# Performance work log

Hardware: AMD Instinct MI355X
Metric: run time of the kernel (lower is better)

## Reference

```python
import jax, jax.numpy as jnp
import numpy as np

B, S, D = 4, 2048, 1024
NEG = -1e10

def setup_inputs() -> dict:
    key = jax.random.key(0)
    ks = jax.random.split(key, 8)
    scale = 1.0 / np.sqrt(D)
    return {
        "hidden_states": jax.random.normal(ks[0], (B, S, D), jnp.float32),
        "mask": jax.random.randint(ks[1], (B, S), 0, 2, jnp.int32),
        "Wq": jax.random.normal(ks[2], (D, D), jnp.float32) * scale,
        "bq": jnp.zeros((D,), jnp.float32),
        "Wk": jax.random.normal(ks[3], (D, D), jnp.float32) * scale,
        "bk": jnp.zeros((D,), jnp.float32),
        "Wv": jax.random.normal(ks[4], (D, D), jnp.float32) * scale,
        "bv": jnp.zeros((D,), jnp.float32),
        "Wo": jax.random.normal(ks[5], (D, D), jnp.float32) * scale,
        "bo": jnp.zeros((D,), jnp.float32),
    }

def reference(hidden_states, mask, Wq, bq, Wk, bk, Wv, bv, Wo, bo):
    # torch Linear: y = x @ W.T + b
    q = jnp.einsum('bsd,ed->bse', hidden_states, Wq) + bq
    k = jnp.einsum('bsd,ed->bse', hidden_states, Wk) + bk
    v = jnp.einsum('bsd,ed->bse', hidden_states, Wv) + bv
    inv_sqrt_d = jnp.asarray(int(hidden_states.shape[-1]) ** (-0.5), hidden_states.dtype)
    weight = jnp.einsum('bqd,bkd->bqk', q, k) * inv_sqrt_d  # [B,S,S]
    # mask viewed as [B,1,S]: key-padding mask broadcast over query dim
    m = mask.reshape(mask.shape[0], 1, mask.shape[1])
    weight = jnp.where(m == 0, jnp.asarray(NEG, weight.dtype), weight)
    a = jax.nn.softmax(weight, axis=-1)
    hid = jnp.einsum('bqk,bkd->bqd', a, v)
    hid_o = jnp.einsum('bsd,ed->bse', hid, Wo) + bo
    return hidden_states + hid_o  # residual=True
```

## Files before the change

### kernel.cpp

```cpp
#include <hip/hip_runtime.h>
#include <stdint.h>


typedef __attribute__((ext_vector_type(8))) short bf16x8;
typedef __attribute__((ext_vector_type(4))) float f32x4;

typedef __attribute__((address_space(3))) void lds_void_t;
typedef __attribute__((address_space(1))) const void glb_void_t;

__device__ __forceinline__ ushort f2bf(float f) {
  uint32_t u = __float_as_uint(f);
  u += 0x7FFF + ((u >> 16) & 1);
  return (ushort)(u >> 16);
}
__device__ __forceinline__ float bf2f(ushort u) {
  return __uint_as_float(((uint32_t)u) << 16);
}

__global__ __launch_bounds__(256) void convert_all(
    const float* __restrict__ X, const float* __restrict__ Wq,
    const float* __restrict__ Wk, const float* __restrict__ Wv,
    const float* __restrict__ Wo, const float* __restrict__ bq,
    const float* __restrict__ bk,
    ushort* __restrict__ Xb, ushort* __restrict__ Wqb, ushort* __restrict__ Wkb,
    ushort* __restrict__ Wvb, ushort* __restrict__ Wob,
    float* __restrict__ bqk) {
  if (blockIdx.x >= 12288) {
#pragma unroll
    for (int u = 0; u < 2; ++u) {
      int idx4 = threadIdx.x * 2 + u;
      int base = idx4 * 4;
      float4 v = (base < 1024) ? *(const float4*)(bq + base)
                               : *(const float4*)(bk + base - 1024);
      *(float4*)(bqk + base) = v;
    }
    return;
  }
  int64_t i = (int64_t)blockIdx.x * blockDim.x + threadIdx.x;
  int64_t o4 = i * 4;
  const float* s; ushort* d; int64_t off;
  if (o4 < 8388608)        { s = X;  d = Xb;  off = o4; }
  else if (o4 < 9437184)   { s = Wq; d = Wqb; off = o4 - 8388608; }
  else if (o4 < 10485760)  { s = Wk; d = Wkb; off = o4 - 9437184; }
  else if (o4 < 11534336)  { s = Wv; d = Wvb; off = o4 - 10485760; }
  else                     { s = Wo; d = Wob; off = o4 - 11534336; }
  float4 v = *(const float4*)(s + off);
  ushort4 o;
  o.x = f2bf(v.x); o.y = f2bf(v.y); o.z = f2bf(v.z); o.w = f2bf(v.w);
  *(ushort4*)(d + off) = o;
}


#define BAR   __builtin_amdgcn_s_barrier()
#define SCHED __builtin_amdgcn_sched_barrier(0)
#define LGKM0 asm volatile("s_waitcnt lgkmcnt(0)" ::: "memory")
#define VMC(n) asm volatile("s_waitcnt vmcnt(" #n ")" ::: "memory")

#define ST(gp, loff, BUFBASE)                                                  \
  do {                                                                         \
    __builtin_amdgcn_global_load_lds((glb_void_t*)(gp),                        \
                                     (lds_void_t*)((BUFBASE) + (loff)), 16, 0, 0); \
    (gp) += 64;                                                                \
  } while (0)

template <int MODE>
__global__ __launch_bounds__(512, 2) void gemm8(
    const ushort* __restrict__ Ag, const ushort* __restrict__ Bg,
    void* __restrict__ Og, const float* __restrict__ bias,
    const float* __restrict__ resid,
    int N, int K, int lda, int ldb, int ldo,
    long long sAz, long long sBz, long long sOz, float scale) {
  __shared__ ushort As0[16384], As1[16384], Bs0[8192], Bs1[8192];

  const int z = blockIdx.z;
  const ushort* A = Ag + (int64_t)z * sAz;
  const ushort* B = Bg + (int64_t)z * sBz;

  const int tilesN = N >> 7;
  const int nwg = gridDim.x;
  const int q8 = nwg >> 3, r8 = nwg & 7;
  const int xcd = blockIdx.x & 7, sub = blockIdx.x >> 3;
  const int wg = (xcd < r8 ? xcd * (q8 + 1) : r8 * (q8 + 1) + (xcd - r8) * q8) + sub;
  const int tm = wg / tilesN, tn = wg % tilesN;

  const int tid = threadIdx.x;
  const int wid = tid >> 6;
  const int lane = tid & 63;
  const int lr = lane & 15;
  const int kq = lane >> 4;
  const int wr = (wid >> 1) * 64;
  const int wc = (wid & 1) * 64;

  const int64_t abase = (int64_t)tm * 256;
  const int64_t bbase = (int64_t)tn * 128;

  const int idxA0 = tid, idxA1 = 512 + tid, idxA2 = 1024 + tid, idxA3 = 1536 + tid;
  const int idxB0 = tid, idxB1 = 512 + tid;

  const int rA0 = idxA0 >> 3, rA1 = idxA1 >> 3, rA2 = idxA2 >> 3, rA3 = idxA3 >> 3;
  const int rB0 = idxB0 >> 3, rB1 = idxB1 >> 3;

  const ushort* gA0 = A + (abase + rA0) * lda + ((idxA0 & 7) ^ (rA0 & 7)) * 8;
  const ushort* gA1 = A + (abase + rA1) * lda + ((idxA1 & 7) ^ (rA1 & 7)) * 8;
  const ushort* gA2 = A + (abase + rA2) * lda + ((idxA2 & 7) ^ (rA2 & 7)) * 8;
  const ushort* gA3 = A + (abase + rA3) * lda + ((idxA3 & 7) ^ (rA3 & 7)) * 8;
  const ushort* gB0 = B + (bbase + rB0) * ldb + ((idxB0 & 7) ^ (rB0 & 7)) * 8;
  const ushort* gB1 = B + (bbase + rB1) * ldb + ((idxB1 & 7) ^ (rB1 & 7)) * 8;

  const int lA0 = idxA0 * 8, lA1 = idxA1 * 8, lA2 = idxA2 * 8, lA3 = idxA3 * 8;
  const int lB0 = idxB0 * 8, lB1 = idxB1 * 8;

  const int rsw0 = (kq ^ (lr & 7)) * 8;
  const int rsw1 = rsw0 ^ 32;
  const ushort* Arp0 = As0 + (wr + lr) * 64;
  const ushort* Arp1 = As1 + (wr + lr) * 64;
  const ushort* Brp0 = Bs0 + (wc + lr) * 64;
  const ushort* Brp1 = Bs1 + (wc + lr) * 64;

  bf16x8 a[4][2], b[4][2];
  f32x4 acc[4][4];
#pragma unroll
  for (int m = 0; m < 4; ++m)
#pragma unroll
    for (int n = 0; n < 4; ++n) acc[m][n] = (f32x4){0.f, 0.f, 0.f, 0.f};

#define RD_A(BUF, mi)                                                    \
  {                                                                      \
    const ushort* p_ = (BUF ? Arp1 : Arp0) + (mi) * 1024;                \
    a[mi][0] = *(const bf16x8*)(p_ + rsw0);                              \
    a[mi][1] = *(const bf16x8*)(p_ + rsw1);                              \
  }
#define RD_B(BUF, ni)                                                    \
  {                                                                      \
    const ushort* p_ = (BUF ? Brp1 : Brp0) + (ni) * 1024;                \
    b[ni][0] = *(const bf16x8*)(p_ + rsw0);                              \
    b[ni][1] = *(const bf16x8*)(p_ + rsw1);                              \
  }
#define MFMA2(mi, ni)                                                                   \
  acc[mi][ni] = __builtin_amdgcn_mfma_f32_16x16x32_bf16(a[mi][0], b[ni][0], acc[mi][ni], 0, 0, 0); \
  acc[mi][ni] = __builtin_amdgcn_mfma_f32_16x16x32_bf16(a[mi][1], b[ni][1], acc[mi][ni], 0, 0, 0);
#define QUAD(m0_, n0_)                                                   \
  __builtin_amdgcn_s_setprio(1);                                         \
  MFMA2(m0_, n0_) MFMA2(m0_, n0_ + 1) MFMA2(m0_ + 1, n0_) MFMA2(m0_ + 1, n0_ + 1) \
  __builtin_amdgcn_s_setprio(0);

  ST(gA0, lA0, As0); ST(gA1, lA1, As0); ST(gA2, lA2, As0); ST(gA3, lA3, As0);
  ST(gB0, lB0, Bs0); ST(gB1, lB1, Bs0);
  ST(gA0, lA0, As1); ST(gA1, lA1, As1); ST(gA2, lA2, As1); ST(gA3, lA3, As1);
  ST(gB0, lB0, Bs1); ST(gB1, lB1, Bs1);
  VMC(6); BAR; SCHED;

  const int NI = K >> 7;
  for (int i = 0; i < NI; ++i) {
    const bool last = (i == NI - 1);
    RD_A(0, 0) RD_A(0, 1) RD_B(0, 0) RD_B(0, 1)
    BAR; LGKM0; SCHED;
    QUAD(0, 0)
    SCHED; BAR;
    RD_B(0, 2) RD_B(0, 3)
    BAR; LGKM0; SCHED;
    QUAD(0, 2)
    SCHED; BAR;
    RD_A(0, 2) RD_A(0, 3)
    BAR; LGKM0; SCHED;
    QUAD(2, 2)
    SCHED; BAR;
    if (!last) { ST(gA0, lA0, As0); ST(gA1, lA1, As0); }
    BAR; SCHED;
    QUAD(2, 0)
    SCHED;
    if (last) { VMC(0); } else { VMC(2); }
    BAR;
    RD_A(1, 0) RD_A(1, 1) RD_B(1, 0) RD_B(1, 1)
    if (!last) { ST(gA2, lA2, As0); ST(gA3, lA3, As0); }
    BAR; LGKM0; SCHED;
    QUAD(0, 0)
    SCHED; BAR;
    RD_A(1, 2) RD_A(1, 3) RD_B(1, 2) RD_B(1, 3)
    if (!last) { ST(gB0, lB0, Bs0); ST(gB1, lB1, Bs0); }
    BAR; LGKM0; SCHED;
    QUAD(0, 2)
    SCHED; BAR;
    if (!last) { ST(gA0, lA0, As1); ST(gA1, lA1, As1); ST(gA2, lA2, As1); ST(gA3, lA3, As1); }
    BAR; SCHED;
    QUAD(2, 2)
    SCHED; BAR;
    if (!last) { ST(gB0, lB0, Bs1); ST(gB1, lB1, Bs1); }
    BAR; SCHED;
    QUAD(2, 0)
    SCHED;
    if (!last) { VMC(6); }
    BAR;
  }

#pragma unroll
  for (int m = 0; m < 4; ++m) {
#pragma unroll
    for (int n = 0; n < 4; ++n) {
      int c = tn * 128 + wc + n * 16 + lr;
      int r0 = tm * 256 + wr + m * 16 + kq * 4;
#pragma unroll
      for (int i = 0; i < 4; ++i) {
        int rrow = r0 + i;
        float v = acc[m][n][i];
        int64_t oo = (int64_t)z * sOz + (int64_t)rrow * ldo + c;
        if constexpr (MODE == 0) {
          v += bias[c];
          ((ushort*)Og)[oo] = f2bf(v);
        } else if constexpr (MODE == 1) {
          v += bias[rrow];
          ((ushort*)Og)[oo] = f2bf(v);
        } else if constexpr (MODE == 2) {
          v *= scale;
          ((ushort*)Og)[oo] = f2bf(v);
        } else {
          v += bias[c] + resid[(int64_t)rrow * ldo + c];
          ((float*)Og)[oo] = v;
        }
      }
    }
  }
#undef RD_A
#undef RD_B
#undef MFMA2
#undef QUAD
}

__global__ __launch_bounds__(256) void softmax_rows(ushort* __restrict__ P,
                                                    const int* __restrict__ mask) {
  const int row = blockIdx.x;
  const int b = row >> 11;
  ushort* prow = P + (int64_t)row * 2048;
  const int* mrow = mask + (b << 11);
  const int tid = threadIdx.x;
  const int wid = tid >> 6, lane = tid & 63;

  float v[8];
#pragma unroll
  for (int t = 0; t < 2; ++t) {
    int c4 = t * 256 + tid;
    ushort4 pv = *(const ushort4*)(prow + c4 * 4);
    int4 mv = *(const int4*)(mrow + c4 * 4);
    v[t * 4 + 0] = mv.x ? bf2f(pv.x) : -1e10f;
    v[t * 4 + 1] = mv.y ? bf2f(pv.y) : -1e10f;
    v[t * 4 + 2] = mv.z ? bf2f(pv.z) : -1e10f;
    v[t * 4 + 3] = mv.w ? bf2f(pv.w) : -1e10f;
  }
  float mx = -3e38f;
#pragma unroll
  for (int j = 0; j < 8; ++j) mx = fmaxf(mx, v[j]);
#pragma unroll
  for (int off = 32; off; off >>= 1) mx = fmaxf(mx, __shfl_xor(mx, off));
  __shared__ float redm[4];
  __shared__ float reds[4];
  if (lane == 0) redm[wid] = mx;
  __syncthreads();
  mx = fmaxf(fmaxf(redm[0], redm[1]), fmaxf(redm[2], redm[3]));

  float e[8];
  float s = 0.f;
#pragma unroll
  for (int j = 0; j < 8; ++j) {
    e[j] = __expf(v[j] - mx);
    s += e[j];
  }
#pragma unroll
  for (int off = 32; off; off >>= 1) s += __shfl_xor(s, off);
  if (lane == 0) reds[wid] = s;
  __syncthreads();
  s = reds[0] + reds[1] + reds[2] + reds[3];
  float inv = 1.0f / s;

#pragma unroll
  for (int t = 0; t < 2; ++t) {
    int c4 = t * 256 + tid;
    ushort4 o;
    o.x = f2bf(e[t * 4 + 0] * inv);
    o.y = f2bf(e[t * 4 + 1] * inv);
    o.z = f2bf(e[t * 4 + 2] * inv);
    o.w = f2bf(e[t * 4 + 3] * inv);
    *(ushort4*)(prow + c4 * 4) = o;
  }
}

extern "C" void kernel_launch(void* const* d_in, const int* in_sizes, int n_in,
                              void* d_out, int out_size, void* d_ws, size_t ws_size,
                              hipStream_t stream) {
  const float* hs = (const float*)d_in[0];
  const int* mask = (const int*)d_in[1];
  const float* Wq = (const float*)d_in[2];
  const float* bq = (const float*)d_in[3];
  const float* Wk = (const float*)d_in[4];
  const float* bk = (const float*)d_in[5];
  const float* Wv = (const float*)d_in[6];
  const float* bv = (const float*)d_in[7];
  const float* Wo = (const float*)d_in[8];
  const float* bo = (const float*)d_in[9];
  float* out = (float*)d_out;
  char* w = (char*)d_ws;

  ushort* Xb   = (ushort*)(w + 0);
  ushort* Wqb  = (ushort*)(w + 16777216);
  ushort* Wkb  = (ushort*)(w + 18874368);
  ushort* Wvb  = (ushort*)(w + 20971520);
  ushort* Wob  = (ushort*)(w + 23068672);
  ushort* QKb  = (ushort*)(w + 25165824);
  ushort* Vt   = (ushort*)(w + 58720256);
  ushort* P    = (ushort*)(w + 75497472);
  float*  bqk  = (float*)(w + 75497472);
  ushort* AO   = (ushort*)(w + 109051904);

  convert_all<<<12289, 256, 0, stream>>>(hs, Wq, Wk, Wv, Wo, bq, bk,
                                         Xb, Wqb, Wkb, Wvb, Wob, bqk);

  gemm8<0><<<dim3(512, 1, 1), 512, 0, stream>>>(Xb, Wqb, QKb, bqk, nullptr,
      2048, 1024, 1024, 1024, 2048, 0, 0, 0, 1.f);

  gemm8<1><<<dim3(256, 1, 1), 512, 0, stream>>>(Wvb, Xb, Vt, bv, nullptr,
      8192, 1024, 1024, 1024, 8192, 0, 0, 0, 1.f);

  gemm8<2><<<dim3(128, 1, 4), 512, 0, stream>>>(QKb, QKb + 1024, P, nullptr, nullptr,
      2048, 1024, 2048, 2048, 2048,
      (long long)2048 * 2048, (long long)2048 * 2048, (long long)2048 * 2048,
      0.03125f);

  softmax_rows<<<8192, 256, 0, stream>>>(P, mask);

  gemm8<2><<<dim3(64, 1, 4), 512, 0, stream>>>(P, Vt, AO, nullptr, nullptr,
      1024, 2048, 2048, 8192, 1024,
      (long long)2048 * 2048, (long long)2048, (long long)2048 * 1024, 1.f);

  gemm8<3><<<dim3(256, 1, 1), 512, 0, stream>>>(AO, Wob, (void*)out, bo, hs,
      1024, 1024, 1024, 1024, 1024, 0, 0, 0, 1.f);
}
```

Measured before the change: 215.9 us.

## Enlarge GEMM tiles to 256-wide N with per-GEMM wave-count template

Reworks the bf16 MFMA GEMM so each block computes a 256-column tile. A new WM template parameter picks 8 waves (256x256 tile) or 4 waves (128x256 tile), and each wave now owns a 128x64 sub-tile with a doubled accumulator array. The load/compute pipeline is reorganised to match, and the launch grids are resized per GEMM. The aim is more operand reuse per byte loaded from global memory and LDS. The cost is higher register and LDS use (128KB of LDS for the WM=2 variant), fewer blocks per launch and lower occupancy.

```diff
diff --git a/kernel.cpp b/kernel.cpp
--- a/kernel.cpp
+++ b/kernel.cpp
@@ -54,29 +54,25 @@
 #define BAR   __builtin_amdgcn_s_barrier()
 #define SCHED __builtin_amdgcn_sched_barrier(0)
 #define LGKM0 asm volatile("s_waitcnt lgkmcnt(0)" ::: "memory")
-#define VMC(n) asm volatile("s_waitcnt vmcnt(" #n ")" ::: "memory")
-
-#define ST(gp, loff, BUFBASE)                                                  \
-  do {                                                                         \
-    __builtin_amdgcn_global_load_lds((glb_void_t*)(gp),                        \
-                                     (lds_void_t*)((BUFBASE) + (loff)), 16, 0, 0); \
-    (gp) += 64;                                                                \
-  } while (0)
-
-template <int MODE>
-__global__ __launch_bounds__(512, 2) void gemm8(
+#define VMC0  asm volatile("s_waitcnt vmcnt(0)" ::: "memory")
+
+template <int MODE, int WM>
+__global__ __launch_bounds__(WM * 256, WM) void gemm8(
     const ushort* __restrict__ Ag, const ushort* __restrict__ Bg,
     void* __restrict__ Og, const float* __restrict__ bias,
     const float* __restrict__ resid,
     int N, int K, int lda, int ldb, int ldo,
     long long sAz, long long sBz, long long sOz, float scale) {
-  __shared__ ushort As0[16384], As1[16384], Bs0[8192], Bs1[8192];
+  constexpr int THREADS = WM * 256;
+  constexpr int BM = WM * 128;
+  __shared__ ushort As[2][BM * 64];
+  __shared__ ushort Bs[2][256 * 64];
 
   const int z = blockIdx.z;
   const ushort* A = Ag + (int64_t)z * sAz;
   const ushort* B = Bg + (int64_t)z * sBz;
 
-  const int tilesN = N >> 7;
+  const int tilesN = N >> 8;
   const int nwg = gridDim.x;
   const int q8 = nwg >> 3, r8 = nwg & 7;
   const int xcd = blockIdx.x & 7, sub = blockIdx.x >> 3;
@@ -88,117 +84,137 @@
   const int lane = tid & 63;
   const int lr = lane & 15;
   const int kq = lane >> 4;
-  const int wr = (wid >> 1) * 64;
-  const int wc = (wid & 1) * 64;
-
-  const int64_t abase = (int64_t)tm * 256;
-  const int64_t bbase = (int64_t)tn * 128;
-
-  const int idxA0 = tid, idxA1 = 512 + tid, idxA2 = 1024 + tid, idxA3 = 1536 + tid;
-  const int idxB0 = tid, idxB1 = 512 + tid;
-
-  const int rA0 = idxA0 >> 3, rA1 = idxA1 >> 3, rA2 = idxA2 >> 3, rA3 = idxA3 >> 3;
-  const int rB0 = idxB0 >> 3, rB1 = idxB1 >> 3;
-
-  const ushort* gA0 = A + (abase + rA0) * lda + ((idxA0 & 7) ^ (rA0 & 7)) * 8;
-  const ushort* gA1 = A + (abase + rA1) * lda + ((idxA1 & 7) ^ (rA1 & 7)) * 8;
-  const ushort* gA2 = A + (abase + rA2) * lda + ((idxA2 & 7) ^ (rA2 & 7)) * 8;
-  const ushort* gA3 = A + (abase + rA3) * lda + ((idxA3 & 7) ^ (rA3 & 7)) * 8;
-  const ushort* gB0 = B + (bbase + rB0) * ldb + ((idxB0 & 7) ^ (rB0 & 7)) * 8;
-  const ushort* gB1 = B + (bbase + rB1) * ldb + ((idxB1 & 7) ^ (rB1 & 7)) * 8;
-
-  const int lA0 = idxA0 * 8, lA1 = idxA1 * 8, lA2 = idxA2 * 8, lA3 = idxA3 * 8;
-  const int lB0 = idxB0 * 8, lB1 = idxB1 * 8;
+  const int wr = (WM == 2) ? (wid >> 2) * 128 : 0;
+  const int wc = (wid & 3) * 64;
+
+  const int64_t abase = (int64_t)tm * BM;
+  const int64_t bbase = (int64_t)tn * 256;
+
+#define MKA(s_) (A + (abase + (((s_)*THREADS + tid) >> 3)) * lda + \
+                 ((((s_)*THREADS + tid) & 7) ^ ((((s_)*THREADS + tid) >> 3) & 7)) * 8)
+#define MKB(s_) (B + (bbase + (((s_)*THREADS + tid) >> 3)) * ldb + \
+                 ((((s_)*THREADS + tid) & 7) ^ ((((s_)*THREADS + tid) >> 3) & 7)) * 8)
+  const ushort* gA0 = MKA(0); const ushort* gA1 = MKA(1);
+  const ushort* gA2 = MKA(2); const ushort* gA3 = MKA(3);
+  const ushort* gB0 = MKB(0); const ushort* gB1 = MKB(1);
+  const ushort* gB2 = MKB(2); const ushort* gB3 = MKB(3);
+  const ushort* gB4 = nullptr; const ushort* gB5 = nullptr;
+  const ushort* gB6 = nullptr; const ushort* gB7 = nullptr;
+  if constexpr (WM == 1) { gB4 = MKB(4); gB5 = MKB(5); gB6 = MKB(6); gB7 = MKB(7); }
+#undef MKA
+#undef MKB
+
+#define ST_A(s_, BUF) do { \
+    __builtin_amdgcn_global_load_lds((glb_void_t*)gA##s_, \
+      (lds_void_t*)((char*)&As[BUF][0] + ((s_) * THREADS + tid) * 16), 16, 0, 0); \
+    gA##s_ += 64; } while (0)
+#define ST_B(s_, BUF) do { \
+    __builtin_amdgcn_global_load_lds((glb_void_t*)gB##s_, \
+      (lds_void_t*)((char*)&Bs[BUF][0] + ((s_) * THREADS + tid) * 16), 16, 0, 0); \
+    gB##s_ += 64; } while (0)
+#define STAGE_BH0(BUF) do { \
+    if constexpr (WM == 2) { ST_B(0, BUF); ST_B(1, BUF); } \
+    else { ST_B(0, BUF); ST_B(1, BUF); ST_B(2, BUF); ST_B(3, BUF); } } while (0)
+#define STAGE_BH1(BUF) do { \
+    if constexpr (WM == 2) { ST_B(2, BUF); ST_B(3, BUF); } \
+    else { ST_B(4, BUF); ST_B(5, BUF); ST_B(6, BUF); ST_B(7, BUF); } } while (0)
+#define VMCG do { \
+    if constexpr (WM == 2) { asm volatile("s_waitcnt vmcnt(4)" ::: "memory"); } \
+    else { asm volatile("s_waitcnt vmcnt(8)" ::: "memory"); } } while (0)
 
   const int rsw0 = (kq ^ (lr & 7)) * 8;
   const int rsw1 = rsw0 ^ 32;
-  const ushort* Arp0 = As0 + (wr + lr) * 64;
-  const ushort* Arp1 = As1 + (wr + lr) * 64;
-  const ushort* Brp0 = Bs0 + (wc + lr) * 64;
-  const ushort* Brp1 = Bs1 + (wc + lr) * 64;
+  const ushort* Arp0 = &As[0][(wr + lr) * 64];
+  const ushort* Arp1 = &As[1][(wr + lr) * 64];
+  const ushort* Brp0 = &Bs[0][(wc + lr) * 64];
+  const ushort* Brp1 = &Bs[1][(wc + lr) * 64];
 
   bf16x8 a[4][2], b[4][2];
-  f32x4 acc[4][4];
-#pragma unroll
-  for (int m = 0; m < 4; ++m)
+  f32x4 acc[8][4];
+#pragma unroll
+  for (int m = 0; m < 8; ++m)
 #pragma unroll
     for (int n = 0; n < 4; ++n) acc[m][n] = (f32x4){0.f, 0.f, 0.f, 0.f};
 
-#define RD_A(BUF, mi)                                                    \
-  {                                                                      \
-    const ushort* p_ = (BUF ? Arp1 : Arp0) + (mi) * 1024;                \
-    a[mi][0] = *(const bf16x8*)(p_ + rsw0);                              \
-    a[mi][1] = *(const bf16x8*)(p_ + rsw1);                              \
-  }
-#define RD_B(BUF, ni)                                                    \
-  {                                                                      \
-    const ushort* p_ = (BUF ? Brp1 : Brp0) + (ni) * 1024;                \
-    b[ni][0] = *(const bf16x8*)(p_ + rsw0);                              \
-    b[ni][1] = *(const bf16x8*)(p_ + rsw1);                              \
-  }
-#define MFMA2(mi, ni)                                                                   \
-  acc[mi][ni] = __builtin_amdgcn_mfma_f32_16x16x32_bf16(a[mi][0], b[ni][0], acc[mi][ni], 0, 0, 0); \
-  acc[mi][ni] = __builtin_amdgcn_mfma_f32_16x16x32_bf16(a[mi][1], b[ni][1], acc[mi][ni], 0, 0, 0);
-#define QUAD(m0_, n0_)                                                   \
-  __builtin_amdgcn_s_setprio(1);                                         \
-  MFMA2(m0_, n0_) MFMA2(m0_, n0_ + 1) MFMA2(m0_ + 1, n0_) MFMA2(m0_ + 1, n0_ + 1) \
-  __builtin_amdgcn_s_setprio(0);
-
-  ST(gA0, lA0, As0); ST(gA1, lA1, As0); ST(gA2, lA2, As0); ST(gA3, lA3, As0);
-  ST(gB0, lB0, Bs0); ST(gB1, lB1, Bs0);
-  ST(gA0, lA0, As1); ST(gA1, lA1, As1); ST(gA2, lA2, As1); ST(gA3, lA3, As1);
-  ST(gB0, lB0, Bs1); ST(gB1, lB1, Bs1);
-  VMC(6); BAR; SCHED;
+#define RD_A4(BUF, mb) { \
+    const ushort* p_ = (BUF ? Arp1 : Arp0) + (mb) * 1024; \
+    a[0][0] = *(const bf16x8*)(p_ + rsw0);        a[0][1] = *(const bf16x8*)(p_ + rsw1); \
+    a[1][0] = *(const bf16x8*)(p_ + 1024 + rsw0); a[1][1] = *(const bf16x8*)(p_ + 1024 + rsw1); \
+    a[2][0] = *(const bf16x8*)(p_ + 2048 + rsw0); a[2][1] = *(const bf16x8*)(p_ + 2048 + rsw1); \
+    a[3][0] = *(const bf16x8*)(p_ + 3072 + rsw0); a[3][1] = *(const bf16x8*)(p_ + 3072 + rsw1); }
+#define RD_B2(BUF, nb) { \
+    const ushort* p_ = (BUF ? Brp1 : Brp0) + (nb) * 1024; \
+    b[nb][0]     = *(const bf16x8*)(p_ + rsw0);        b[nb][1]     = *(const bf16x8*)(p_ + rsw1); \
+    b[nb + 1][0] = *(const bf16x8*)(p_ + 1024 + rsw0); b[nb + 1][1] = *(const bf16x8*)(p_ + 1024 + rsw1); }
+#define MM2(mi, ni, mg, ng) \
+    acc[mg][ng] = __builtin_amdgcn_mfma_f32_16x16x32_bf16(a[mi][0], b[ni][0], acc[mg][ng], 0, 0, 0); \
+    acc[mg][ng] = __builtin_amdgcn_mfma_f32_16x16x32_bf16(a[mi][1], b[ni][1], acc[mg][ng], 0, 0, 0);
+#define CLUSTER(mb, nb) \
+    __builtin_amdgcn_s_setprio(1); \
+    MM2(0, nb, mb + 0, nb) MM2(0, nb + 1, mb + 0, nb + 1) \
+    MM2(1, nb, mb + 1, nb) MM2(1, nb + 1, mb + 1, nb + 1) \
+    MM2(2, nb, mb + 2, nb) MM2(2, nb + 1, mb + 2, nb + 1) \
+    MM2(3, nb, mb + 3, nb) MM2(3, nb + 1, mb + 3, nb + 1) \
+    __builtin_amdgcn_s_setprio(0);
+
+  ST_A(0, 0); ST_A(1, 0); ST_A(2, 0); ST_A(3, 0);
+  STAGE_BH0(0); STAGE_BH1(0);
+  STAGE_BH0(1); STAGE_BH1(1);
+  VMCG; BAR; SCHED;
 
   const int NI = K >> 7;
-  for (int i = 0; i < NI; ++i) {
-    const bool last = (i == NI - 1);
-    RD_A(0, 0) RD_A(0, 1) RD_B(0, 0) RD_B(0, 1)
-    BAR; LGKM0; SCHED;
-    QUAD(0, 0)
-    SCHED; BAR;
-    RD_B(0, 2) RD_B(0, 3)
-    BAR; LGKM0; SCHED;
-    QUAD(0, 2)
-    SCHED; BAR;
-    RD_A(0, 2) RD_A(0, 3)
-    BAR; LGKM0; SCHED;
-    QUAD(2, 2)
-    SCHED; BAR;
-    if (!last) { ST(gA0, lA0, As0); ST(gA1, lA1, As0); }
+  for (int it = 0; it < NI; ++it) {
+    const bool last = (it == NI - 1);
+    RD_A4(0, 0) RD_B2(0, 0)
+    ST_A(0, 1); ST_A(1, 1);
+    BAR; LGKM0; SCHED;
+    CLUSTER(0, 0)
+    SCHED; BAR;
+    RD_B2(0, 2)
+    ST_A(2, 1); ST_A(3, 1);
+    BAR; LGKM0; SCHED;
+    CLUSTER(0, 2)
+    SCHED; BAR;
+    RD_A4(0, 4)
+    if (!last) { STAGE_BH0(0); }
+    BAR; LGKM0; SCHED;
+    CLUSTER(4, 2)
+    SCHED; BAR;
+    if (!last) { STAGE_BH1(0); }
     BAR; SCHED;
-    QUAD(2, 0)
+    CLUSTER(4, 0)
     SCHED;
-    if (last) { VMC(0); } else { VMC(2); }
+    if (last) { VMC0; } else { VMCG; }
     BAR;
-    RD_A(1, 0) RD_A(1, 1) RD_B(1, 0) RD_B(1, 1)
-    if (!last) { ST(gA2, lA2, As0); ST(gA3, lA3, As0); }
-    BAR; LGKM0; SCHED;
-    QUAD(0, 0)
-    SCHED; BAR;
-    RD_A(1, 2) RD_A(1, 3) RD_B(1, 2) RD_B(1, 3)
-    if (!last) { ST(gB0, lB0, Bs0); ST(gB1, lB1, Bs0); }
-    BAR; LGKM0; SCHED;
-    QUAD(0, 2)
-    SCHED; BAR;
-    if (!last) { ST(gA0, lA0, As1); ST(gA1, lA1, As1); ST(gA2, lA2, As1); ST(gA3, lA3, As1); }
+    RD_A4(1, 0) RD_B2(1, 0)
+    if (!last) { ST_A(0, 0); ST_A(1, 0); }
+    BAR; LGKM0; SCHED;
+    CLUSTER(0, 0)
+    SCHED; BAR;
+    RD_B2(1, 2)
+    if (!last) { ST_A(2, 0); ST_A(3, 0); }
+    BAR; LGKM0; SCHED;
+    CLUSTER(0, 2)
+    SCHED; BAR;
+    RD_A4(1, 4)
+    if (!last) { STAGE_BH0(1); }
+    BAR; LGKM0; SCHED;
+    CLUSTER(4, 2)
+    SCHED; BAR;
+    if (!last) { STAGE_BH1(1); }
     BAR; SCHED;
-    QUAD(2, 2)
-    SCHED; BAR;
-    if (!last) { ST(gB0, lB0, Bs1); ST(gB1, lB1, Bs1); }
-    BAR; SCHED;
-    QUAD(2, 0)
+    CLUSTER(4, 0)
     SCHED;
-    if (!last) { VMC(6); }
+    if (!last) { VMCG; }
     BAR;
   }
 
 #pragma unroll
-  for (int m = 0; m < 4; ++m) {
+  for (int m = 0; m < 8; ++m) {
 #pragma unroll
     for (int n = 0; n < 4; ++n) {
-      int c = tn * 128 + wc + n * 16 + lr;
-      int r0 = tm * 256 + wr + m * 16 + kq * 4;
+      int c = tn * 256 + wc + n * 16 + lr;
+      int r0 = tm * BM + wr + m * 16 + kq * 4;
 #pragma unroll
       for (int i = 0; i < 4; ++i) {
         int rrow = r0 + i;
@@ -220,10 +236,15 @@
       }
     }
   }
-#undef RD_A
-#undef RD_B
-#undef MFMA2
-#undef QUAD
+#undef RD_A4
+#undef RD_B2
+#undef MM2
+#undef CLUSTER
+#undef ST_A
+#undef ST_B
+#undef STAGE_BH0
+#undef STAGE_BH1
+#undef VMCG
 }
 
 __global__ __launch_bounds__(256) void softmax_rows(ushort* __restrict__ P,
@@ -313,23 +334,23 @@
   convert_all<<<12289, 256, 0, stream>>>(hs, Wq, Wk, Wv, Wo, bq, bk,
                                          Xb, Wqb, Wkb, Wvb, Wob, bqk);
 
-  gemm8<0><<<dim3(512, 1, 1), 512, 0, stream>>>(Xb, Wqb, QKb, bqk, nullptr,
+  gemm8<0, 2><<<dim3(256, 1, 1), 512, 0, stream>>>(Xb, Wqb, QKb, bqk, nullptr,
       2048, 1024, 1024, 1024, 2048, 0, 0, 0, 1.f);
 
-  gemm8<1><<<dim3(256, 1, 1), 512, 0, stream>>>(Wvb, Xb, Vt, bv, nullptr,
+  gemm8<1, 1><<<dim3(256, 1, 1), 256, 0, stream>>>(Wvb, Xb, Vt, bv, nullptr,
       8192, 1024, 1024, 1024, 8192, 0, 0, 0, 1.f);
 
-  gemm8<2><<<dim3(128, 1, 4), 512, 0, stream>>>(QKb, QKb + 1024, P, nullptr, nullptr,
+  gemm8<2, 2><<<dim3(64, 1, 4), 512, 0, stream>>>(QKb, QKb + 1024, P, nullptr, nullptr,
       2048, 1024, 2048, 2048, 2048,
       (long long)2048 * 2048, (long long)2048 * 2048, (long long)2048 * 2048,
       0.03125f);
 
   softmax_rows<<<8192, 256, 0, stream>>>(P, mask);
 
-  gemm8<2><<<dim3(64, 1, 4), 512, 0, stream>>>(P, Vt, AO, nullptr, nullptr,
+  gemm8<2, 1><<<dim3(64, 1, 4), 256, 0, stream>>>(P, Vt, AO, nullptr, nullptr,
       1024, 2048, 2048, 8192, 1024,
       (long long)2048 * 2048, (long long)2048, (long long)2048 * 1024, 1.f);
 
-  gemm8<3><<<dim3(256, 1, 1), 512, 0, stream>>>(AO, Wob, (void*)out, bo, hs,
+  gemm8<3, 1><<<dim3(256, 1, 1), 256, 0, stream>>>(AO, Wob, (void*)out, bo, hs,
       1024, 1024, 1024, 1024, 1024, 0, 0, 0, 1.f);
 }
```

Result: slower. 229.9 us (+6.5%).
